# Performance work log

Measured on AMD Instinct MI355X. Metric: run time of the kernel, lower is better.

Reference implementation:

```python
import jax, jax.numpy as jnp
import numpy as np

N = 50000
E = 800000
F_IN = 512
H = 128
K = 10
ALPHA = 0.1
EPS = 1e-5  # BatchNorm eps


def setup_inputs() -> dict:
    key = jax.random.key(0)
    ks = jax.random.split(key, 16)
    x = jax.random.normal(ks[0], (N, F_IN), dtype=jnp.float32)
    edge_index = jax.random.randint(ks[1], (2, E), 0, N, dtype=jnp.int64)
    # Linear weights (xavier-ish scale)
    W1 = jax.random.normal(ks[2], (F_IN, H), dtype=jnp.float32) * (1.0 / np.sqrt(F_IN))
    b1 = jnp.zeros((H,), dtype=jnp.float32)
    W2 = jax.random.normal(ks[3], (H, H), dtype=jnp.float32) * (1.0 / np.sqrt(H))
    b2 = jnp.zeros((H,), dtype=jnp.float32)
    # BatchNorm (eval mode: running stats)
    gamma1 = jnp.ones((H,), dtype=jnp.float32)
    beta1 = jnp.zeros((H,), dtype=jnp.float32)
    mean1 = jax.random.normal(ks[4], (H,), dtype=jnp.float32) * 0.1
    var1 = jax.random.uniform(ks[5], (H,), dtype=jnp.float32) + 0.5
    gamma2 = jnp.ones((H,), dtype=jnp.float32)
    beta2 = jnp.zeros((H,), dtype=jnp.float32)
    mean2 = jax.random.normal(ks[6], (H,), dtype=jnp.float32) * 0.1
    var2 = jax.random.uniform(ks[7], (H,), dtype=jnp.float32) + 0.5
    return {
        "x": x, "edge_index": edge_index,
        "W1": W1, "b1": b1, "gamma1": gamma1, "beta1": beta1, "mean1": mean1, "var1": var1,
        "W2": W2, "b2": b2, "gamma2": gamma2, "beta2": beta2, "mean2": mean2, "var2": var2,
    }


def _bn_eval(h, gamma, beta, mean, var):
    return (h - mean) * jax.lax.rsqrt(var + EPS) * gamma + beta


def _appnp_prop(h, edge_index):
    # add self loops
    loop = jnp.arange(N, dtype=edge_index.dtype)
    src = jnp.concatenate([edge_index[0], loop])
    dst = jnp.concatenate([edge_index[1], loop])
    # symmetric GCN normalization: deg^{-1/2}[src] * deg^{-1/2}[dst]
    deg = jax.ops.segment_sum(jnp.ones_like(src, dtype=h.dtype), dst, num_segments=N)
    dinv = jax.lax.rsqrt(jnp.maximum(deg, 1.0))
    norm = dinv[src] * dinv[dst]  # [E+N]
    h0 = h

    def step(carry, _):
        msg = carry[src] * norm[:, None]                    # [E+N, H]
        agg = jax.ops.segment_sum(msg, dst, num_segments=N)  # [N, H]
        return (1.0 - ALPHA) * agg + ALPHA * h0, None

    out, _ = jax.lax.scan(step, h, None, length=K)
    return out


def reference(x, edge_index, W1, b1, gamma1, beta1, mean1, var1,
              W2, b2, gamma2, beta2, mean2, var2):
    h = jax.nn.relu(x @ W1 + b1)
    h = _bn_eval(h, gamma1, beta1, mean1, var1)
    # dropout inactive (eval mode)
    h = h @ W2 + b2
    h = _bn_eval(h, gamma2, beta2, mean2, var2)
    return _appnp_prop(h, edge_index)
```

## Files before the change

### kernel.cpp

```cpp
#include <hip/hip_runtime.h>

#define ALPHA_F 0.1f
#define EPS_F   1e-5f

typedef __bf16 bf16_t;
typedef __bf16 bf16x8 __attribute__((ext_vector_type(8)));
typedef float  f32x4  __attribute__((ext_vector_type(4)));
typedef unsigned short u16x8 __attribute__((ext_vector_type(8)));
typedef _Float16 h16x4 __attribute__((ext_vector_type(4)));
typedef _Float16 h16x8 __attribute__((ext_vector_type(8)));

__device__ __forceinline__ int pad_cnt(int d) { return (d + 8) & ~7; }

__global__ void convert_wt(const float* __restrict__ W,
                           bf16_t* __restrict__ hi, bf16_t* __restrict__ lo, int K)
{
    int idx = blockIdx.x * 256 + threadIdx.x;
    if (idx < K * 128) {
        int k = idx >> 7, n = idx & 127;
        float f  = W[idx];
        bf16_t h = (bf16_t)f;
        hi[(size_t)n * K + k] = h;
        lo[(size_t)n * K + k] = (bf16_t)(f - (float)h);
    }
}

template<bool A_HALF, bool OUT_HALF>
__global__ __launch_bounds__(256) void gemm_mfma_bn(
    const void* __restrict__ Av,
    const bf16_t* __restrict__ Wthi, const bf16_t* __restrict__ Wtlo,
    const float* __restrict__ bias,
    const float* __restrict__ gamma, const float* __restrict__ beta,
    const float* __restrict__ mean,  const float* __restrict__ var,
    void* __restrict__ outv, int M, int K, int do_relu)
{
    __shared__ __align__(16) unsigned short WH[128][40];
    __shared__ __align__(16) unsigned short WL[128][40];

    const int t   = threadIdx.x;
    const int w   = t >> 6;
    const int l   = t & 63;
    const int l15 = l & 15;
    const int lk  = l >> 4;
    const int bm  = blockIdx.x * 64;
    const int r   = bm + w * 16 + l15;
    const int nk  = K >> 5;

    const float*    Af = (const float*)Av;
    const _Float16* Ah = (const _Float16*)Av;

    const bf16_t* Wsrc = ((t < 128) ? Wthi : Wtlo) + (size_t)(t & 127) * K;
    unsigned short* Wdst = (t < 128) ? &WH[t & 127][0] : &WL[t & 127][0];

    f32x4 acc[8];
#pragma unroll
    for (int f = 0; f < 8; ++f) acc[f] = (f32x4){0.f, 0.f, 0.f, 0.f};

    float a_cur[8], a_nxt[8];
    u16x8 wreg[4], wreg_n[4];

    auto loadA = [&](int kbase, float* dstv) {
        if (r < M) {
            if (A_HALF) {
                h16x8 v = *(const h16x8*)(Ah + (size_t)r * K + kbase + lk * 8);
#pragma unroll
                for (int j = 0; j < 8; ++j) dstv[j] = (float)v[j];
            } else {
                f32x4 v0 = *(const f32x4*)(Af + (size_t)r * K + kbase + lk * 8);
                f32x4 v1 = *(const f32x4*)(Af + (size_t)r * K + kbase + lk * 8 + 4);
#pragma unroll
                for (int j = 0; j < 4; ++j) { dstv[j] = v0[j]; dstv[4 + j] = v1[j]; }
            }
        } else {
#pragma unroll
            for (int j = 0; j < 8; ++j) dstv[j] = 0.f;
        }
    };

#pragma unroll
    for (int c = 0; c < 4; ++c) wreg[c] = *(const u16x8*)(Wsrc + c * 8);
    loadA(0, a_cur);

    for (int i = 0; i < nk; ++i) {
#pragma unroll
        for (int c = 0; c < 4; ++c) *(u16x8*)&Wdst[c * 8] = wreg[c];

        const int kn = (i + 1) << 5;
        if (kn < K) {
#pragma unroll
            for (int c = 0; c < 4; ++c) wreg_n[c] = *(const u16x8*)(Wsrc + kn + c * 8);
            loadA(kn, a_nxt);
        }
        __syncthreads();

        bf16x8 ahi, alo;
#pragma unroll
        for (int j = 0; j < 8; ++j) {
            float  f0 = a_cur[j];
            bf16_t h0 = (bf16_t)f0;
            ahi[j] = h0;
            alo[j] = (bf16_t)(f0 - (float)h0);
        }
#pragma unroll
        for (int f = 0; f < 8; ++f) {
            u16x8 uh = *(const u16x8*)&WH[f * 16 + l15][lk * 8];
            u16x8 ul = *(const u16x8*)&WL[f * 16 + l15][lk * 8];
            bf16x8 wh = __builtin_bit_cast(bf16x8, uh);
            bf16x8 wl = __builtin_bit_cast(bf16x8, ul);
            acc[f] = __builtin_amdgcn_mfma_f32_16x16x32_bf16(ahi, wh, acc[f], 0, 0, 0);
            acc[f] = __builtin_amdgcn_mfma_f32_16x16x32_bf16(alo, wh, acc[f], 0, 0, 0);
            acc[f] = __builtin_amdgcn_mfma_f32_16x16x32_bf16(ahi, wl, acc[f], 0, 0, 0);
        }
        __syncthreads();
#pragma unroll
        for (int j = 0; j < 8; ++j) a_cur[j] = a_nxt[j];
#pragma unroll
        for (int c = 0; c < 4; ++c) wreg[c] = wreg_n[c];
    }

#pragma unroll
    for (int f = 0; f < 8; ++f) {
        int col  = f * 16 + l15;
        float s  = gamma[col] * rsqrtf(var[col] + EPS_F);
        float sh = beta[col] - mean[col] * s;
        float bb = bias[col];
#pragma unroll
        for (int rr = 0; rr < 4; ++rr) {
            int rg = bm + w * 16 + lk * 4 + rr;
            if (rg < M) {
                float v = acc[f][rr] + bb;
                if (do_relu) v = fmaxf(v, 0.f);
                v = v * s + sh;
                if (OUT_HALF) ((_Float16*)outv)[(size_t)rg * 128 + col] = (_Float16)v;
                else          ((float*)outv)[(size_t)rg * 128 + col]    = v;
            }
        }
    }
}

__global__ void count_deg(const int* __restrict__ dst, int E, int* __restrict__ deg)
{
    int e = blockIdx.x * 256 + threadIdx.x;
    if (e < E) atomicAdd(&deg[dst[e]], 1);
}

__global__ __launch_bounds__(256) void scan_block_sums(
    const int* __restrict__ deg, int* __restrict__ bsum, int N)
{
    __shared__ int sh[256];
    const int t  = threadIdx.x;
    const int i0 = blockIdx.x * 1024 + t * 4;
    int s = 0;
    if (i0 + 3 < N) {
        int4 d4 = *(const int4*)(deg + i0);
        s = pad_cnt(d4.x) + pad_cnt(d4.y) + pad_cnt(d4.z) + pad_cnt(d4.w);
    } else {
#pragma unroll
        for (int j = 0; j < 4; ++j)
            if (i0 + j < N) s += pad_cnt(deg[i0 + j]);
    }
    sh[t] = s;
    __syncthreads();
#pragma unroll
    for (int d = 128; d > 0; d >>= 1) {
        if (t < d) sh[t] += sh[t + d];
        __syncthreads();
    }
    if (t == 0) bsum[blockIdx.x] = sh[0];
}

__global__ __launch_bounds__(256) void scan_offsets(
    const int* __restrict__ deg, const int* __restrict__ bsum,
    int* __restrict__ offs, int* __restrict__ cursor, int N, int B)
{
    __shared__ int sh[256];
    __shared__ int sbase;
    const int b = blockIdx.x, t = threadIdx.x;

    int v = (t < b && t < B) ? bsum[t] : 0;
    sh[t] = v;
    __syncthreads();
#pragma unroll
    for (int d = 128; d > 0; d >>= 1) {
        if (t < d) sh[t] += sh[t + d];
        __syncthreads();
    }
    if (t == 0) sbase = sh[0];
    __syncthreads();

    const int i0 = b * 1024 + t * 4;
    int c[4], s = 0;
#pragma unroll
    for (int j = 0; j < 4; ++j) {
        int i = i0 + j;
        c[j] = (i < N) ? pad_cnt(deg[i]) : 0;
        s += c[j];
    }
    sh[t] = s;
    __syncthreads();
    for (int d = 1; d < 256; d <<= 1) {
        int o = (t >= d) ? sh[t - d] : 0;
        __syncthreads();
        sh[t] += o;
        __syncthreads();
    }
    int run = sbase + sh[t] - s;
#pragma unroll
    for (int j = 0; j < 4; ++j) {
        int i = i0 + j;
        if (i < N) {
            offs[i]   = run;
            cursor[i] = run;
            run += c[j];
        }
    }
    if (b == B - 1 && t == 255) offs[N] = run;
}

__global__ void compute_dinv(const int* __restrict__ deg, float* __restrict__ dinv, int N)
{
    int i = blockIdx.x * 256 + threadIdx.x;
    if (i < N) dinv[i] = rsqrtf((float)(deg[i] + 1));
}

__global__ void scatter_csr(const int* __restrict__ src, const int* __restrict__ dst,
                            int E, const float* __restrict__ dinv,
                            int* __restrict__ cursor,
                            int* __restrict__ csr_src, float* __restrict__ csr_val)
{
    int e = blockIdx.x * 256 + threadIdx.x;
    if (e < E) {
        int s = src[e], d = dst[e];
        int pos = atomicAdd(&cursor[d], 1);
        csr_src[pos] = s;
        csr_val[pos] = dinv[s] * dinv[d];
    }
}

__global__ void fill_self_pad(const int* __restrict__ offs, const int* __restrict__ deg,
                              const float* __restrict__ dinv,
                              int* __restrict__ csr_src, float* __restrict__ csr_val, int N)
{
    int i = blockIdx.x * 256 + threadIdx.x;
    if (i < N) {
        int base = offs[i], d = deg[i], end = offs[i + 1];
        float di = dinv[i];
        csr_src[base + d] = i;
        csr_val[base + d] = di * di;
        for (int p = base + d + 1; p < end; ++p) {
            csr_src[p] = i;
            csr_val[p] = 0.f;
        }
    }
}

__global__ __launch_bounds__(256) void appnp_step(
    const _Float16* __restrict__ cur, const _Float16* __restrict__ h0,
    const int* __restrict__ offs,
    const int* __restrict__ csr_src, const float* __restrict__ csr_val,
    _Float16* __restrict__ nxt, float* __restrict__ fout, int N)
{
    int wv = (int)((blockIdx.x * 256u + threadIdx.x) >> 6);
    if (wv >= N) return;
    const int i    = __builtin_amdgcn_readfirstlane(wv);
    const int lane = (int)(threadIdx.x & 63u);
    const int g    = lane >> 4;
    const int fl   = (lane & 15) * 8;

    int e   = offs[i];
    int end = offs[i + 1];

    f32x4 accL = (f32x4){0.f, 0.f, 0.f, 0.f};
    f32x4 accH = (f32x4){0.f, 0.f, 0.f, 0.f};

    int   iA = csr_src[e + g],     iB = csr_src[e + 4 + g];
    float wA = csr_val[e + g],     wB = csr_val[e + 4 + g];
    h16x8 vA = *(const h16x8*)(cur + (size_t)iA * 128 + fl);
    h16x8 vB = *(const h16x8*)(cur + (size_t)iB * 128 + fl);

    for (e += 8; e < end; e += 8) {
        int   iA2 = csr_src[e + g],     iB2 = csr_src[e + 4 + g];
        float wA2 = csr_val[e + g],     wB2 = csr_val[e + 4 + g];
        h16x8 vA2 = *(const h16x8*)(cur + (size_t)iA2 * 128 + fl);
        h16x8 vB2 = *(const h16x8*)(cur + (size_t)iB2 * 128 + fl);
#pragma unroll
        for (int j = 0; j < 4; ++j) {
            accL[j] = fmaf(wA, (float)vA[j],     accL[j]);
            accH[j] = fmaf(wA, (float)vA[4 + j], accH[j]);
            accL[j] = fmaf(wB, (float)vB[j],     accL[j]);
            accH[j] = fmaf(wB, (float)vB[4 + j], accH[j]);
        }
        wA = wA2; wB = wB2; vA = vA2; vB = vB2;
    }
#pragma unroll
    for (int j = 0; j < 4; ++j) {
        accL[j] = fmaf(wA, (float)vA[j],     accL[j]);
        accH[j] = fmaf(wA, (float)vA[4 + j], accH[j]);
        accL[j] = fmaf(wB, (float)vB[j],     accL[j]);
        accH[j] = fmaf(wB, (float)vB[4 + j], accH[j]);
    }

#pragma unroll
    for (int j = 0; j < 4; ++j) {
        accL[j] += __shfl_xor(accL[j], 16);
        accL[j] += __shfl_xor(accL[j], 32);
        accH[j] += __shfl_xor(accH[j], 16);
        accH[j] += __shfl_xor(accH[j], 32);
    }

    if (lane < 16) {
        h16x8 hv = *(const h16x8*)(h0 + (size_t)i * 128 + fl);
        float o[8];
#pragma unroll
        for (int j = 0; j < 4; ++j) {
            o[j]     = ALPHA_F * (float)hv[j]     + (1.f - ALPHA_F) * accL[j];
            o[4 + j] = ALPHA_F * (float)hv[4 + j] + (1.f - ALPHA_F) * accH[j];
        }
        if (fout) {
            f32x4 o0, o1;
#pragma unroll
            for (int j = 0; j < 4; ++j) { o0[j] = o[j]; o1[j] = o[4 + j]; }
            *(f32x4*)(fout + (size_t)i * 128 + fl)     = o0;
            *(f32x4*)(fout + (size_t)i * 128 + fl + 4) = o1;
        } else {
            h16x8 o16;
#pragma unroll
            for (int j = 0; j < 8; ++j) o16[j] = (_Float16)o[j];
            *(h16x8*)(nxt + (size_t)i * 128 + fl) = o16;
        }
    }
}

static inline size_t align_up(size_t x) { return (x + 255) & ~(size_t)255; }

extern "C" void kernel_launch(void* const* d_in, const int* in_sizes, int n_in,
                              void* d_out, int out_size, void* d_ws, size_t ws_size,
                              hipStream_t stream)
{
    const float* x   = (const float*)d_in[0];
    const int*   ei  = (const int*)d_in[1];
    const float* W1  = (const float*)d_in[2];
    const float* b1  = (const float*)d_in[3];
    const float* g1  = (const float*)d_in[4];
    const float* be1 = (const float*)d_in[5];
    const float* m1  = (const float*)d_in[6];
    const float* v1  = (const float*)d_in[7];
    const float* W2  = (const float*)d_in[8];
    const float* b2  = (const float*)d_in[9];
    const float* g2  = (const float*)d_in[10];
    const float* be2 = (const float*)d_in[11];
    const float* m2  = (const float*)d_in[12];
    const float* v2  = (const float*)d_in[13];

    const int N = in_sizes[0] / 512;
    const int E = in_sizes[1] / 2;
    const int* src = ei;
    const int* dst = ei + E;
    const int CSR_CAP = E + 8 * N;
    const int NB = (N + 1023) / 1024;

    char* ws = (char*)d_ws;
    size_t off = 0;
    _Float16* hAh = (_Float16*)(ws + off); off += align_up((size_t)N * 128 * 2);
    _Float16* h0h = (_Float16*)(ws + off); off += align_up((size_t)N * 128 * 2);
    _Float16* p0  = (_Float16*)(ws + off); off += align_up((size_t)N * 128 * 2);
    _Float16* p1  = (_Float16*)(ws + off); off += align_up((size_t)N * 128 * 2);
    int*    deg  = (int*)(ws + off);    off += align_up((size_t)N * 4);
    float*  dinv = (float*)(ws + off);  off += align_up((size_t)N * 4);
    int*    offs = (int*)(ws + off);    off += align_up((size_t)(N + 1) * 4);
    int*    curs = (int*)(ws + off);    off += align_up((size_t)N * 4);
    int*    bsum = (int*)(ws + off);    off += align_up((size_t)256 * 4);
    int*    csrs = (int*)(ws + off);    off += align_up((size_t)CSR_CAP * 4);
    float*  csrv = (float*)(ws + off);  off += align_up((size_t)CSR_CAP * 4);
    bf16_t* w1h  = (bf16_t*)(ws + off); off += align_up((size_t)512 * 128 * 2);
    bf16_t* w1l  = (bf16_t*)(ws + off); off += align_up((size_t)512 * 128 * 2);
    bf16_t* w2h  = (bf16_t*)(ws + off); off += align_up((size_t)128 * 128 * 2);
    bf16_t* w2l  = (bf16_t*)(ws + off); off += align_up((size_t)128 * 128 * 2);

    hipMemsetAsync(deg, 0, (size_t)N * 4, stream);
    count_deg<<<(E + 255) / 256, 256, 0, stream>>>(dst, E, deg);
    scan_block_sums<<<NB, 256, 0, stream>>>(deg, bsum, N);
    scan_offsets<<<NB, 256, 0, stream>>>(deg, bsum, offs, curs, N, NB);
    compute_dinv<<<(N + 255) / 256, 256, 0, stream>>>(deg, dinv, N);
    scatter_csr<<<(E + 255) / 256, 256, 0, stream>>>(src, dst, E, dinv, curs, csrs, csrv);
    fill_self_pad<<<(N + 255) / 256, 256, 0, stream>>>(offs, deg, dinv, csrs, csrv, N);

    convert_wt<<<(512 * 128 + 255) / 256, 256, 0, stream>>>(W1, w1h, w1l, 512);
    convert_wt<<<(128 * 128 + 255) / 256, 256, 0, stream>>>(W2, w2h, w2l, 128);

    gemm_mfma_bn<false, true><<<(N + 63) / 64, 256, 0, stream>>>(
        x, w1h, w1l, b1, g1, be1, m1, v1, hAh, N, 512, 1);
    gemm_mfma_bn<true, true><<<(N + 63) / 64, 256, 0, stream>>>(
        hAh, w2h, w2l, b2, g2, be2, m2, v2, h0h, N, 128, 0);

    const _Float16* cur = h0h;
    for (int k = 0; k < 10; ++k) {
        _Float16* nxt = (k & 1) ? p1 : p0;
        float* fo = (k == 9) ? (float*)d_out : nullptr;
        appnp_step<<<(N + 3) / 4, 256, 0, stream>>>(
            cur, h0h, offs, csrs, csrv, nxt, fo, N);
        cur = nxt;
    }

    (void)n_in; (void)out_size; (void)ws_size;
}
```

Baseline: 494.1 us.

## Switch GEMMs to single fp16 MFMA with register-direct weights; deepen SpMM prefetch

The GEMMs drop the three-pass bf16 hi/lo split in favour of a single fp16 MFMA pass. Weights are loaded straight from global memory into registers, replacing the LDS staging and barriers, and the K loop is unrolled to 64 per step. This cuts MFMA work by about 3x and removes synchronisation, at the cost of fp16 precision on x and the weights. The APPNP gather loop now prefetches edge indices and weights two steps ahead, with a padded CSR tail so those reads stay in bounds.

Result: slower. 529.6 us (+7.2%).

```diff
diff --git a/kernel.cpp b/kernel.cpp
--- a/kernel.cpp
+++ b/kernel.cpp
@@ -3,40 +3,31 @@
 #define ALPHA_F 0.1f
 #define EPS_F   1e-5f
 
-typedef __bf16 bf16_t;
-typedef __bf16 bf16x8 __attribute__((ext_vector_type(8)));
-typedef float  f32x4  __attribute__((ext_vector_type(4)));
+typedef float    f32x4 __attribute__((ext_vector_type(4)));
+typedef _Float16 h16x8 __attribute__((ext_vector_type(8)));
 typedef unsigned short u16x8 __attribute__((ext_vector_type(8)));
-typedef _Float16 h16x4 __attribute__((ext_vector_type(4)));
-typedef _Float16 h16x8 __attribute__((ext_vector_type(8)));
 
 __device__ __forceinline__ int pad_cnt(int d) { return (d + 8) & ~7; }
 
-__global__ void convert_wt(const float* __restrict__ W,
-                           bf16_t* __restrict__ hi, bf16_t* __restrict__ lo, int K)
+__global__ void convert_wt16(const float* __restrict__ W,
+                             _Float16* __restrict__ Wt, int K)
 {
     int idx = blockIdx.x * 256 + threadIdx.x;
     if (idx < K * 128) {
         int k = idx >> 7, n = idx & 127;
-        float f  = W[idx];
-        bf16_t h = (bf16_t)f;
-        hi[(size_t)n * K + k] = h;
-        lo[(size_t)n * K + k] = (bf16_t)(f - (float)h);
+        Wt[(size_t)n * K + k] = (_Float16)W[idx];
     }
 }
 
 template<bool A_HALF, bool OUT_HALF>
 __global__ __launch_bounds__(256) void gemm_mfma_bn(
     const void* __restrict__ Av,
-    const bf16_t* __restrict__ Wthi, const bf16_t* __restrict__ Wtlo,
+    const _Float16* __restrict__ Wt,
     const float* __restrict__ bias,
     const float* __restrict__ gamma, const float* __restrict__ beta,
     const float* __restrict__ mean,  const float* __restrict__ var,
     void* __restrict__ outv, int M, int K, int do_relu)
 {
-    __shared__ __align__(16) unsigned short WH[128][40];
-    __shared__ __align__(16) unsigned short WL[128][40];
-
     const int t   = threadIdx.x;
     const int w   = t >> 6;
     const int l   = t & 63;
@@ -44,78 +35,65 @@
     const int lk  = l >> 4;
     const int bm  = blockIdx.x * 64;
     const int r   = bm + w * 16 + l15;
-    const int nk  = K >> 5;
-
-    const float*    Af = (const float*)Av;
-    const _Float16* Ah = (const _Float16*)Av;
-
-    const bf16_t* Wsrc = ((t < 128) ? Wthi : Wtlo) + (size_t)(t & 127) * K;
-    unsigned short* Wdst = (t < 128) ? &WH[t & 127][0] : &WL[t & 127][0];
+    const size_t arow = (size_t)((r < M) ? r : 0) * K;
+
+    const float*    Af = (const float*)Av    + arow;
+    const _Float16* Ah = (const _Float16*)Av + arow;
 
     f32x4 acc[8];
 #pragma unroll
     for (int f = 0; f < 8; ++f) acc[f] = (f32x4){0.f, 0.f, 0.f, 0.f};
 
-    float a_cur[8], a_nxt[8];
-    u16x8 wreg[4], wreg_n[4];
-
-    auto loadA = [&](int kbase, float* dstv) {
-        if (r < M) {
+    h16x8 aC[2], aN[2];
+    h16x8 bC[2][8], bN[2][8];
+
+    auto loadA = [&](int k0, h16x8* dst) {
+#pragma unroll
+        for (int s = 0; s < 2; ++s) {
             if (A_HALF) {
-                h16x8 v = *(const h16x8*)(Ah + (size_t)r * K + kbase + lk * 8);
-#pragma unroll
-                for (int j = 0; j < 8; ++j) dstv[j] = (float)v[j];
+                dst[s] = *(const h16x8*)(Ah + k0 + s * 32 + lk * 8);
             } else {
-                f32x4 v0 = *(const f32x4*)(Af + (size_t)r * K + kbase + lk * 8);
-                f32x4 v1 = *(const f32x4*)(Af + (size_t)r * K + kbase + lk * 8 + 4);
-#pragma unroll
-                for (int j = 0; j < 4; ++j) { dstv[j] = v0[j]; dstv[4 + j] = v1[j]; }
+                f32x4 v0 = *(const f32x4*)(Af + k0 + s * 32 + lk * 8);
+                f32x4 v1 = *(const f32x4*)(Af + k0 + s * 32 + lk * 8 + 4);
+                h16x8 h;
+#pragma unroll
+                for (int j = 0; j < 4; ++j) {
+                    h[j]     = (_Float16)v0[j];
+                    h[4 + j] = (_Float16)v1[j];
+                }
+                dst[s] = h;
             }
-        } else {
-#pragma unroll
-            for (int j = 0; j < 8; ++j) dstv[j] = 0.f;
         }
     };
-
-#pragma unroll
-    for (int c = 0; c < 4; ++c) wreg[c] = *(const u16x8*)(Wsrc + c * 8);
-    loadA(0, a_cur);
-
-    for (int i = 0; i < nk; ++i) {
-#pragma unroll
-        for (int c = 0; c < 4; ++c) *(u16x8*)&Wdst[c * 8] = wreg[c];
-
-        const int kn = (i + 1) << 5;
-        if (kn < K) {
-#pragma unroll
-            for (int c = 0; c < 4; ++c) wreg_n[c] = *(const u16x8*)(Wsrc + kn + c * 8);
-            loadA(kn, a_nxt);
-        }
-        __syncthreads();
-
-        bf16x8 ahi, alo;
-#pragma unroll
-        for (int j = 0; j < 8; ++j) {
-            float  f0 = a_cur[j];
-            bf16_t h0 = (bf16_t)f0;
-            ahi[j] = h0;
-            alo[j] = (bf16_t)(f0 - (float)h0);
-        }
-#pragma unroll
-        for (int f = 0; f < 8; ++f) {
-            u16x8 uh = *(const u16x8*)&WH[f * 16 + l15][lk * 8];
-            u16x8 ul = *(const u16x8*)&WL[f * 16 + l15][lk * 8];
-            bf16x8 wh = __builtin_bit_cast(bf16x8, uh);
-            bf16x8 wl = __builtin_bit_cast(bf16x8, ul);
-            acc[f] = __builtin_amdgcn_mfma_f32_16x16x32_bf16(ahi, wh, acc[f], 0, 0, 0);
-            acc[f] = __builtin_amdgcn_mfma_f32_16x16x32_bf16(alo, wh, acc[f], 0, 0, 0);
-            acc[f] = __builtin_amdgcn_mfma_f32_16x16x32_bf16(ahi, wl, acc[f], 0, 0, 0);
-        }
-        __syncthreads();
-#pragma unroll
-        for (int j = 0; j < 8; ++j) a_cur[j] = a_nxt[j];
-#pragma unroll
-        for (int c = 0; c < 4; ++c) wreg[c] = wreg_n[c];
+    auto loadB = [&](int k0, h16x8 (*dst)[8]) {
+#pragma unroll
+        for (int s = 0; s < 2; ++s)
+#pragma unroll
+            for (int f = 0; f < 8; ++f)
+                dst[s][f] = *(const h16x8*)(Wt + (size_t)(f * 16 + l15) * K
+                                               + k0 + s * 32 + lk * 8);
+    };
+
+    loadA(0, aC);
+    loadB(0, bC);
+
+    for (int k0 = 0; k0 < K; k0 += 64) {
+        if (k0 + 64 < K) {
+            loadA(k0 + 64, aN);
+            loadB(k0 + 64, bN);
+        }
+#pragma unroll
+        for (int s = 0; s < 2; ++s)
+#pragma unroll
+            for (int f = 0; f < 8; ++f)
+                acc[f] = __builtin_amdgcn_mfma_f32_16x16x32_f16(
+                    aC[s], bC[s][f], acc[f], 0, 0, 0);
+#pragma unroll
+        for (int s = 0; s < 2; ++s) {
+            aC[s] = aN[s];
+#pragma unroll
+            for (int f = 0; f < 8; ++f) bC[s][f] = bN[s][f];
+        }
     }
 
 #pragma unroll
@@ -254,6 +232,15 @@
     }
 }
 
+__global__ void pad_csr_tail(const int* __restrict__ offs, int N,
+                             int* __restrict__ csr_src, float* __restrict__ csr_val)
+{
+    int base = offs[N];
+    int j = threadIdx.x;
+    csr_src[base + j] = 0;
+    csr_val[base + j] = 0.f;
+}
+
 __global__ __launch_bounds__(256) void appnp_step(
     const _Float16* __restrict__ cur, const _Float16* __restrict__ h0,
     const int* __restrict__ offs,
@@ -273,31 +260,34 @@
     f32x4 accL = (f32x4){0.f, 0.f, 0.f, 0.f};
     f32x4 accH = (f32x4){0.f, 0.f, 0.f, 0.f};
 
-    int   iA = csr_src[e + g],     iB = csr_src[e + 4 + g];
-    float wA = csr_val[e + g],     wB = csr_val[e + 4 + g];
-    h16x8 vA = *(const h16x8*)(cur + (size_t)iA * 128 + fl);
-    h16x8 vB = *(const h16x8*)(cur + (size_t)iB * 128 + fl);
-
-    for (e += 8; e < end; e += 8) {
-        int   iA2 = csr_src[e + g],     iB2 = csr_src[e + 4 + g];
-        float wA2 = csr_val[e + g],     wB2 = csr_val[e + 4 + g];
-        h16x8 vA2 = *(const h16x8*)(cur + (size_t)iA2 * 128 + fl);
-        h16x8 vB2 = *(const h16x8*)(cur + (size_t)iB2 * 128 + fl);
+    int   iA0 = csr_src[e + g],     iB0 = csr_src[e + 4 + g];
+    float wA0 = csr_val[e + g],     wB0 = csr_val[e + 4 + g];
+    h16x8 vA  = *(const h16x8*)(cur + (size_t)iA0 * 128 + fl);
+    h16x8 vB  = *(const h16x8*)(cur + (size_t)iB0 * 128 + fl);
+    int   iA1 = csr_src[e + 8 + g],  iB1 = csr_src[e + 12 + g];
+    float wA1 = csr_val[e + 8 + g],  wB1 = csr_val[e + 12 + g];
+
+    for (; e + 8 < end; e += 8) {
+        int   iA2 = csr_src[e + 16 + g], iB2 = csr_src[e + 20 + g];
+        float wA2 = csr_val[e + 16 + g], wB2 = csr_val[e + 20 + g];
+        h16x8 vA1 = *(const h16x8*)(cur + (size_t)iA1 * 128 + fl);
+        h16x8 vB1 = *(const h16x8*)(cur + (size_t)iB1 * 128 + fl);
 #pragma unroll
         for (int j = 0; j < 4; ++j) {
-            accL[j] = fmaf(wA, (float)vA[j],     accL[j]);
-            accH[j] = fmaf(wA, (float)vA[4 + j], accH[j]);
-            accL[j] = fmaf(wB, (float)vB[j],     accL[j]);
-            accH[j] = fmaf(wB, (float)vB[4 + j], accH[j]);
-        }
-        wA = wA2; wB = wB2; vA = vA2; vB = vB2;
+            accL[j] = fmaf(wA0, (float)vA[j],     accL[j]);
+            accH[j] = fmaf(wA0, (float)vA[4 + j], accH[j]);
+            accL[j] = fmaf(wB0, (float)vB[j],     accL[j]);
+            accH[j] = fmaf(wB0, (float)vB[4 + j], accH[j]);
+        }
+        vA = vA1; vB = vB1; wA0 = wA1; wB0 = wB1;
+        iA1 = iA2; iB1 = iB2; wA1 = wA2; wB1 = wB2;
     }
 #pragma unroll
     for (int j = 0; j < 4; ++j) {
-        accL[j] = fmaf(wA, (float)vA[j],     accL[j]);
-        accH[j] = fmaf(wA, (float)vA[4 + j], accH[j]);
-        accL[j] = fmaf(wB, (float)vB[j],     accL[j]);
-        accH[j] = fmaf(wB, (float)vB[4 + j], accH[j]);
+        accL[j] = fmaf(wA0, (float)vA[j],     accL[j]);
+        accH[j] = fmaf(wA0, (float)vA[4 + j], accH[j]);
+        accL[j] = fmaf(wB0, (float)vB[j],     accL[j]);
+        accH[j] = fmaf(wB0, (float)vB[4 + j], accH[j]);
     }
 
 #pragma unroll
@@ -356,7 +346,7 @@
     const int E = in_sizes[1] / 2;
     const int* src = ei;
     const int* dst = ei + E;
-    const int CSR_CAP = E + 8 * N;
+    const int CSR_CAP = E + 8 * N + 64;
     const int NB = (N + 1023) / 1024;
 
     char* ws = (char*)d_ws;
@@ -372,10 +362,8 @@
     int*    bsum = (int*)(ws + off);    off += align_up((size_t)256 * 4);
     int*    csrs = (int*)(ws + off);    off += align_up((size_t)CSR_CAP * 4);
     float*  csrv = (float*)(ws + off);  off += align_up((size_t)CSR_CAP * 4);
-    bf16_t* w1h  = (bf16_t*)(ws + off); off += align_up((size_t)512 * 128 * 2);
-    bf16_t* w1l  = (bf16_t*)(ws + off); off += align_up((size_t)512 * 128 * 2);
-    bf16_t* w2h  = (bf16_t*)(ws + off); off += align_up((size_t)128 * 128 * 2);
-    bf16_t* w2l  = (bf16_t*)(ws + off); off += align_up((size_t)128 * 128 * 2);
+    _Float16* w1t = (_Float16*)(ws + off); off += align_up((size_t)512 * 128 * 2);
+    _Float16* w2t = (_Float16*)(ws + off); off += align_up((size_t)128 * 128 * 2);
 
     hipMemsetAsync(deg, 0, (size_t)N * 4, stream);
     count_deg<<<(E + 255) / 256, 256, 0, stream>>>(dst, E, deg);
@@ -384,14 +372,15 @@
     compute_dinv<<<(N + 255) / 256, 256, 0, stream>>>(deg, dinv, N);
     scatter_csr<<<(E + 255) / 256, 256, 0, stream>>>(src, dst, E, dinv, curs, csrs, csrv);
     fill_self_pad<<<(N + 255) / 256, 256, 0, stream>>>(offs, deg, dinv, csrs, csrv, N);
-
-    convert_wt<<<(512 * 128 + 255) / 256, 256, 0, stream>>>(W1, w1h, w1l, 512);
-    convert_wt<<<(128 * 128 + 255) / 256, 256, 0, stream>>>(W2, w2h, w2l, 128);
+    pad_csr_tail<<<1, 32, 0, stream>>>(offs, N, csrs, csrv);
+
+    convert_wt16<<<(512 * 128 + 255) / 256, 256, 0, stream>>>(W1, w1t, 512);
+    convert_wt16<<<(128 * 128 + 255) / 256, 256, 0, stream>>>(W2, w2t, 128);
 
     gemm_mfma_bn<false, true><<<(N + 63) / 64, 256, 0, stream>>>(
-        x, w1h, w1l, b1, g1, be1, m1, v1, hAh, N, 512, 1);
+        x, w1t, b1, g1, be1, m1, v1, hAh, N, 512, 1);
     gemm_mfma_bn<true, true><<<(N + 63) / 64, 256, 0, stream>>>(
-        hAh, w2h, w2l, b2, g2, be2, m2, v2, h0h, N, 128, 0);
+        hAh, w2t, b2, g2, be2, m2, v2, h0h, N, 128, 0);
 
     const _Float16* cur = h0h;
     for (int k = 0; k < 10; ++k) {
```
